# Kernel optimization log

Measured on AMD Instinct MI355X. Metric: run time of the kernel, lower is better.

The kernel has to match this reference:

```python
import jax, jax.numpy as jnp
import numpy as np

MAX_VAL = 448.0  # FP8 E4M3 max
EPS = 1e-12


def fp8_e4m3_fake_quantize(t):
    """Clamp -> per-tensor scale to E4M3 range -> power-of-two step rounding (3 mantissa bits -> step = 2^exp/8)."""
    clamped = jnp.clip(t, -MAX_VAL, MAX_VAL)
    amax = jnp.maximum(jnp.max(jnp.abs(clamped)), EPS)
    scale = MAX_VAL / amax
    scaled = clamped * scale
    sign = jnp.sign(scaled)
    mag = jnp.maximum(jnp.abs(scaled), EPS)
    exp = jnp.floor(jnp.log2(mag))
    step = jnp.exp2(exp) / 8.0
    quantized = sign * (jnp.round(mag / step) * step)
    return quantized / scale


def setup_inputs() -> dict:
    key = jax.random.key(0)
    kx, kw, kb = jax.random.split(key, 3)
    B, S, IN_F, OUT_F = 4, 2048, 4096, 16384
    x = jax.random.normal(kx, (B, S, IN_F), dtype=jnp.float32)
    weight = jax.random.normal(kw, (OUT_F, IN_F), dtype=jnp.float32) * 0.02
    bias = jax.random.normal(kb, (OUT_F,), dtype=jnp.float32) * 0.02
    return {"x": x, "weight": weight, "bias": bias}


def reference(x, weight, bias):
    w_q = fp8_e4m3_fake_quantize(weight)   # [out_f, in_f]
    x_q = fp8_e4m3_fake_quantize(x)        # [b, s, in_f]
    # F.linear: x_q @ w_q.T + bias
    return jnp.einsum('bsi,oi->bso', x_q, w_q) + bias
```

## Files before the change

### kernel.cpp

```cpp
#include <hip/hip_runtime.h>

typedef __bf16 bf16x8 __attribute__((ext_vector_type(8)));
typedef float f32x4 __attribute__((ext_vector_type(4)));

#define MAXV 448.0f

__device__ __forceinline__ void gld_lds16(const void* g, void* l) {
  __builtin_amdgcn_global_load_lds(
      (const __attribute__((address_space(1))) void*)g,
      (__attribute__((address_space(3))) void*)l, 16, 0, 0);
}

__global__ void init_ws_kernel(unsigned int* p) {
  if (threadIdx.x < 2) p[threadIdx.x] = 0u;
}

__global__ void amax_kernel(const float* __restrict__ in, long n4, unsigned int* out) {
  long i0 = (long)blockIdx.x * blockDim.x + threadIdx.x;
  long stride = (long)gridDim.x * blockDim.x;
  const float4* in4 = (const float4*)in;
  float m = 0.0f;
  for (long i = i0; i < n4; i += stride) {
    float4 v = in4[i];
    m = fmaxf(m, fmaxf(fmaxf(fabsf(v.x), fabsf(v.y)), fmaxf(fabsf(v.z), fabsf(v.w))));
  }
  m = fminf(m, MAXV);
#pragma unroll
  for (int off = 32; off >= 1; off >>= 1)
    m = fmaxf(m, __shfl_xor(m, off, 64));
  if ((threadIdx.x & 63) == 0) atomicMax(out, __float_as_uint(m));
}

__device__ __forceinline__ unsigned short fq1(float v, float scale) {
  float c = fminf(fmaxf(v, -MAXV), MAXV);
  float s = c * scale;
  float mag = fmaxf(fabsf(s), 1e-12f);
  unsigned int u = __float_as_uint(mag);
  unsigned int E = u >> 23;
  float t = __uint_as_float((u & 0x007fffffu) | (130u << 23));
  float r = rintf(t);
  float q = r * __uint_as_float((E - 3u) << 23);
  float res = (s == 0.0f) ? 0.0f : copysignf(q, s);
  return (unsigned short)(__float_as_uint(res) >> 16);
}

__global__ void quant_kernel(const float* __restrict__ in, unsigned short* __restrict__ out,
                             long n4, const unsigned int* __restrict__ amax_p) {
  float amax = fmaxf(__uint_as_float(*amax_p), 1e-12f);
  float scale = MAXV / amax;
  long i0 = (long)blockIdx.x * blockDim.x + threadIdx.x;
  long stride = (long)gridDim.x * blockDim.x;
  const float4* in4 = (const float4*)in;
  ushort4* out4 = (ushort4*)out;
  for (long i = i0; i < n4; i += stride) {
    float4 v = in4[i];
    ushort4 o;
    o.x = fq1(v.x, scale);
    o.y = fq1(v.y, scale);
    o.z = fq1(v.z, scale);
    o.w = fq1(v.w, scale);
    out4[i] = o;
  }
}

#define TM 128
#define TN 128
#define BK 32

__global__ __launch_bounds__(256, 2) void gemm_bt_kernel(
    const unsigned short* __restrict__ A, const unsigned short* __restrict__ B,
    const float* __restrict__ bias, const unsigned int* __restrict__ amax_ws,
    float* __restrict__ C, int M, int N, int K) {
  __shared__ __align__(16) unsigned short As[TM * BK];
  __shared__ __align__(16) unsigned short Bs[TN * BK];

  const int tid = threadIdx.x;
  const int lane = tid & 63;
  const int wave = tid >> 6;
  const int wm = wave >> 1, wn = wave & 1;
  const int bn = blockIdx.x, bm = blockIdx.y;

  const int mfrag = lane & 15;
  const int kq = lane >> 4;

  const int sr = tid >> 2;
  const int sc = (tid & 3) * 8;
  const unsigned short* gA0 = A + (long)(bm * TM + sr) * K + sc;
  const unsigned short* gA1 = A + (long)(bm * TM + 64 + sr) * K + sc;
  const unsigned short* gB0 = B + (long)(bn * TN + sr) * K + sc;
  const unsigned short* gB1 = B + (long)(bn * TN + 64 + sr) * K + sc;
  unsigned short* lA0 = As + tid * 8;
  unsigned short* lA1 = As + (256 + tid) * 8;
  unsigned short* lB0 = Bs + tid * 8;
  unsigned short* lB1 = Bs + (256 + tid) * 8;

  f32x4 acc[4][4] = {};

  for (int k0 = 0; k0 < K; k0 += BK) {
    __syncthreads();
    gld_lds16(gA0 + k0, lA0);
    gld_lds16(gA1 + k0, lA1);
    gld_lds16(gB0 + k0, lB0);
    gld_lds16(gB1 + k0, lB1);
    __syncthreads();

    bf16x8 af[4], bf[4];
#pragma unroll
    for (int i = 0; i < 4; ++i) {
      af[i] = *(const bf16x8*)(As + (wm * 64 + i * 16 + mfrag) * BK + kq * 8);
      bf[i] = *(const bf16x8*)(Bs + (wn * 64 + i * 16 + mfrag) * BK + kq * 8);
    }
#pragma unroll
    for (int i = 0; i < 4; ++i)
#pragma unroll
      for (int j = 0; j < 4; ++j)
        acc[i][j] = __builtin_amdgcn_mfma_f32_16x16x32_bf16(af[i], bf[j], acc[i][j], 0, 0, 0);
  }

  float amx = fmaxf(__uint_as_float(amax_ws[0]), 1e-12f);
  float amw = fmaxf(__uint_as_float(amax_ws[1]), 1e-12f);
  float sx = MAXV / amx, sw = MAXV / amw;
  float inv = 1.0f / (sx * sw);

  const int row_base = bm * TM + wm * 64 + (lane >> 4) * 4;
  const int col_base = bn * TN + wn * 64 + (lane & 15);
#pragma unroll
  for (int i = 0; i < 4; ++i)
#pragma unroll
    for (int j = 0; j < 4; ++j) {
      int col = col_base + j * 16;
      float bv = bias[col];
#pragma unroll
      for (int r = 0; r < 4; ++r) {
        int row = row_base + i * 16 + r;
        C[(long)row * N + col] = acc[i][j][r] * inv + bv;
      }
    }
}

extern "C" void kernel_launch(void* const* d_in, const int* in_sizes, int n_in,
                              void* d_out, int out_size, void* d_ws, size_t ws_size,
                              hipStream_t stream) {
  const float* x = (const float*)d_in[0];
  const float* w = (const float*)d_in[1];
  const float* bias = (const float*)d_in[2];
  float* out = (float*)d_out;

  const long NX = in_sizes[0];
  const long NW = in_sizes[1];
  const int N = in_sizes[2];
  const int K = (int)(NW / N);
  const int M = (int)(NX / K);

  unsigned int* amax = (unsigned int*)d_ws;
  unsigned short* xq = (unsigned short*)((char*)d_ws + 256);
  unsigned short* wq = (unsigned short*)((char*)d_ws + 256 + NX * 2);

  init_ws_kernel<<<1, 64, 0, stream>>>(amax);
  amax_kernel<<<1024, 256, 0, stream>>>(x, NX >> 2, amax + 0);
  amax_kernel<<<2048, 256, 0, stream>>>(w, NW >> 2, amax + 1);
  quant_kernel<<<2048, 256, 0, stream>>>(x, xq, NX >> 2, amax + 0);
  quant_kernel<<<2048, 256, 0, stream>>>(w, wq, NW >> 2, amax + 1);

  dim3 grid(N / TN, M / TM);
  gemm_bt_kernel<<<grid, 256, 0, stream>>>(xq, wq, bias, amax, out, M, N, K);
}
```

Before: 2.319 ms.

## Replace GEMM with 256x256 double-buffered, swizzled-LDS, pipelined MFMA kernel

Replaces the 128x128 single-buffered GEMM with a 256x256 tile, 512-thread kernel. It uses a 64-wide K step, XOR-swizzled LDS layout, double-buffered global-to-LDS loads interleaved with MFMA phases, setprio around compute, and an XCD-aware block remap. The aim is to raise data reuse, hide load latency behind compute and cut LDS bank conflicts. The kernel uses the full 128KB of LDS with heavy register pressure, and its many barriers and hand-tuned waitcnt counts could limit occupancy or introduce hazards.

```diff
diff --git a/kernel.cpp b/kernel.cpp
--- a/kernel.cpp
+++ b/kernel.cpp
@@ -63,78 +63,191 @@
   }
 }
 
-#define TM 128
-#define TN 128
-#define BK 32
-
-__global__ __launch_bounds__(256, 2) void gemm_bt_kernel(
+__global__ __launch_bounds__(512, 2) void gemm256_kernel(
     const unsigned short* __restrict__ A, const unsigned short* __restrict__ B,
     const float* __restrict__ bias, const unsigned int* __restrict__ amax_ws,
     float* __restrict__ C, int M, int N, int K) {
-  __shared__ __align__(16) unsigned short As[TM * BK];
-  __shared__ __align__(16) unsigned short Bs[TN * BK];
+  __shared__ __attribute__((aligned(16))) unsigned char lds[131072];
 
   const int tid = threadIdx.x;
   const int lane = tid & 63;
   const int wave = tid >> 6;
-  const int wm = wave >> 1, wn = wave & 1;
-  const int bn = blockIdx.x, bm = blockIdx.y;
-
-  const int mfrag = lane & 15;
-  const int kq = lane >> 4;
-
-  const int sr = tid >> 2;
-  const int sc = (tid & 3) * 8;
-  const unsigned short* gA0 = A + (long)(bm * TM + sr) * K + sc;
-  const unsigned short* gA1 = A + (long)(bm * TM + 64 + sr) * K + sc;
-  const unsigned short* gB0 = B + (long)(bn * TN + sr) * K + sc;
-  const unsigned short* gB1 = B + (long)(bn * TN + 64 + sr) * K + sc;
-  unsigned short* lA0 = As + tid * 8;
-  unsigned short* lA1 = As + (256 + tid) * 8;
-  unsigned short* lB0 = Bs + tid * 8;
-  unsigned short* lB1 = Bs + (256 + tid) * 8;
-
-  f32x4 acc[4][4] = {};
-
-  for (int k0 = 0; k0 < K; k0 += BK) {
-    __syncthreads();
-    gld_lds16(gA0 + k0, lA0);
-    gld_lds16(gA1 + k0, lA1);
-    gld_lds16(gB0 + k0, lB0);
-    gld_lds16(gB1 + k0, lB1);
-    __syncthreads();
-
-    bf16x8 af[4], bf[4];
-#pragma unroll
-    for (int i = 0; i < 4; ++i) {
-      af[i] = *(const bf16x8*)(As + (wm * 64 + i * 16 + mfrag) * BK + kq * 8);
-      bf[i] = *(const bf16x8*)(Bs + (wn * 64 + i * 16 + mfrag) * BK + kq * 8);
-    }
-#pragma unroll
-    for (int i = 0; i < 4; ++i)
-#pragma unroll
-      for (int j = 0; j < 4; ++j)
-        acc[i][j] = __builtin_amdgcn_mfma_f32_16x16x32_bf16(af[i], bf[j], acc[i][j], 0, 0, 0);
-  }
+  const int wm = wave >> 2, wn = wave & 3;
+  const int mfrag = lane & 15, kq = lane >> 4;
+  const int kxor = (kq * 16) ^ (((mfrag >> 3) & 1) << 5);
+
+  const int nbn = N >> 8;
+  const int wg = (blockIdx.x & 7) * (gridDim.x >> 3) + (blockIdx.x >> 3);
+  const int bm = wg / nbn, bn = wg % nbn;
+
+  const int nT = K >> 6;
+
+  const int cA0 = ((tid >> 8) << 9) + (tid & 255);
+  const int cB0 = ((tid >> 7) << 8) + (tid & 127);
+  const int cAq[2] = {cA0, cA0 + 256};
+  const int cBq[2] = {cB0, cB0 + 128};
+  const unsigned short* sA[2][2];
+  const unsigned short* sB[2][2];
+  int dA[2][2], dB[2][2];
+#pragma unroll
+  for (int q = 0; q < 2; ++q) {
+    {
+      int c = cAq[q], row = (c >> 2) & 127, kb = c >> 9, ch = c & 3;
+      int ko = kb * 32 + ((ch * 8) ^ (((row >> 3) & 1) << 4));
+#pragma unroll
+      for (int l = 0; l < 2; ++l) {
+        sA[q][l] = A + (size_t)(bm * 256 + l * 128 + row) * K + ko;
+        dA[q][l] = l * 16384 + c * 16;
+      }
+    }
+    {
+      int c = cBq[q], row = (c >> 2) & 127, kb = c >> 9, ch = c & 3;
+      int ko = kb * 32 + ((ch * 8) ^ (((row >> 3) & 1) << 4));
+#pragma unroll
+      for (int l = 0; l < 2; ++l) {
+        sB[q][l] = B + (size_t)(bn * 256 + l * 128 + row) * K + ko;
+        dB[q][l] = 32768 + l * 16384 + c * 16;
+      }
+    }
+  }
+
+#define STAGE_A(qq, T2)                                              \
+  do {                                                               \
+    long ko_ = (long)(T2) * 64;                                      \
+    int b2_ = ((T2) & 1) * 65536;                                    \
+    gld_lds16(sA[qq][0] + ko_, lds + b2_ + dA[qq][0]);               \
+    gld_lds16(sA[qq][1] + ko_, lds + b2_ + dA[qq][1]);               \
+  } while (0)
+#define STAGE_B(qq, T2)                                              \
+  do {                                                               \
+    long ko_ = (long)(T2) * 64;                                      \
+    int b2_ = ((T2) & 1) * 65536;                                    \
+    gld_lds16(sB[qq][0] + ko_, lds + b2_ + dB[qq][0]);               \
+    gld_lds16(sB[qq][1] + ko_, lds + b2_ + dB[qq][1]);               \
+  } while (0)
+
+  STAGE_A(0, 0);
+  STAGE_B(0, 0);
+  STAGE_B(1, 0);
+  STAGE_A(1, 0);
+  if (nT > 1) {
+    STAGE_A(0, 1);
+    STAGE_B(0, 1);
+    STAGE_B(1, 1);
+    asm volatile("s_waitcnt vmcnt(6)" ::: "memory");
+  } else {
+    asm volatile("s_waitcnt vmcnt(0)" ::: "memory");
+  }
+  __builtin_amdgcn_s_barrier();
+
+  const unsigned char* ldsA0 = lds + wm * 16384 + mfrag * 64 + kxor;
+  const unsigned char* ldsB0 = lds + 32768 + (wn >> 1) * 16384 + (wn & 1) * 4096 + mfrag * 64 + kxor;
+
+  f32x4 acc[8][4] = {};
+  bf16x8 af[4][2], bf[4][2];
+
+  for (int T = 0; T < nT; ++T) {
+    const unsigned char* pA = ldsA0 + (T & 1) * 65536;
+    const unsigned char* pB = ldsB0 + (T & 1) * 65536;
+
+#pragma unroll
+    for (int i = 0; i < 4; ++i)
+#pragma unroll
+      for (int ks = 0; ks < 2; ++ks)
+        af[i][ks] = *(const bf16x8*)(pA + ks * 8192 + i * 1024);
+#pragma unroll
+    for (int j = 0; j < 2; ++j)
+#pragma unroll
+      for (int ks = 0; ks < 2; ++ks)
+        bf[j][ks] = *(const bf16x8*)(pB + ks * 8192 + j * 1024);
+    if (T + 1 < nT) STAGE_A(1, T + 1);
+    __builtin_amdgcn_s_barrier();
+    __builtin_amdgcn_s_setprio(1);
+#pragma unroll
+    for (int i = 0; i < 4; ++i)
+#pragma unroll
+      for (int j = 0; j < 2; ++j) {
+        acc[i][j] = __builtin_amdgcn_mfma_f32_16x16x32_bf16(af[i][0], bf[j][0], acc[i][j], 0, 0, 0);
+        acc[i][j] = __builtin_amdgcn_mfma_f32_16x16x32_bf16(af[i][1], bf[j][1], acc[i][j], 0, 0, 0);
+      }
+    __builtin_amdgcn_s_setprio(0);
+    __builtin_amdgcn_s_barrier();
+
+#pragma unroll
+    for (int j = 2; j < 4; ++j)
+#pragma unroll
+      for (int ks = 0; ks < 2; ++ks)
+        bf[j][ks] = *(const bf16x8*)(pB + ks * 8192 + j * 1024);
+    if (T + 2 < nT) STAGE_A(0, T + 2);
+    __builtin_amdgcn_s_barrier();
+    __builtin_amdgcn_s_setprio(1);
+#pragma unroll
+    for (int i = 0; i < 4; ++i)
+#pragma unroll
+      for (int j = 2; j < 4; ++j) {
+        acc[i][j] = __builtin_amdgcn_mfma_f32_16x16x32_bf16(af[i][0], bf[j][0], acc[i][j], 0, 0, 0);
+        acc[i][j] = __builtin_amdgcn_mfma_f32_16x16x32_bf16(af[i][1], bf[j][1], acc[i][j], 0, 0, 0);
+      }
+    __builtin_amdgcn_s_setprio(0);
+    __builtin_amdgcn_s_barrier();
+
+#pragma unroll
+    for (int i = 0; i < 4; ++i)
+#pragma unroll
+      for (int ks = 0; ks < 2; ++ks)
+        af[i][ks] = *(const bf16x8*)(pA + ks * 8192 + (i + 4) * 1024);
+    if (T + 2 < nT) STAGE_B(0, T + 2);
+    __builtin_amdgcn_s_barrier();
+    __builtin_amdgcn_s_setprio(1);
+#pragma unroll
+    for (int i = 0; i < 4; ++i)
+#pragma unroll
+      for (int j = 0; j < 2; ++j) {
+        acc[i + 4][j] = __builtin_amdgcn_mfma_f32_16x16x32_bf16(af[i][0], bf[j][0], acc[i + 4][j], 0, 0, 0);
+        acc[i + 4][j] = __builtin_amdgcn_mfma_f32_16x16x32_bf16(af[i][1], bf[j][1], acc[i + 4][j], 0, 0, 0);
+      }
+    __builtin_amdgcn_s_setprio(0);
+    __builtin_amdgcn_s_barrier();
+
+    if (T + 2 < nT) STAGE_B(1, T + 2);
+    if (T < nT - 2) {
+      asm volatile("s_waitcnt vmcnt(6)" ::: "memory");
+    } else {
+      asm volatile("s_waitcnt vmcnt(0)" ::: "memory");
+    }
+    __builtin_amdgcn_s_barrier();
+    __builtin_amdgcn_s_setprio(1);
+#pragma unroll
+    for (int i = 0; i < 4; ++i)
+#pragma unroll
+      for (int j = 2; j < 4; ++j) {
+        acc[i + 4][j] = __builtin_amdgcn_mfma_f32_16x16x32_bf16(af[i][0], bf[j][0], acc[i + 4][j], 0, 0, 0);
+        acc[i + 4][j] = __builtin_amdgcn_mfma_f32_16x16x32_bf16(af[i][1], bf[j][1], acc[i + 4][j], 0, 0, 0);
+      }
+    __builtin_amdgcn_s_setprio(0);
+    __builtin_amdgcn_s_barrier();
+  }
+#undef STAGE_A
+#undef STAGE_B
 
   float amx = fmaxf(__uint_as_float(amax_ws[0]), 1e-12f);
   float amw = fmaxf(__uint_as_float(amax_ws[1]), 1e-12f);
   float sx = MAXV / amx, sw = MAXV / amw;
   float inv = 1.0f / (sx * sw);
 
-  const int row_base = bm * TM + wm * 64 + (lane >> 4) * 4;
-  const int col_base = bn * TN + wn * 64 + (lane & 15);
-#pragma unroll
-  for (int i = 0; i < 4; ++i)
+  const int rb = bm * 256 + wm * 128 + (lane >> 4) * 4;
+  const int cb = bn * 256 + wn * 64 + (lane & 15);
+  float bv[4];
+#pragma unroll
+  for (int j = 0; j < 4; ++j) bv[j] = bias[cb + j * 16];
+#pragma unroll
+  for (int i = 0; i < 8; ++i)
 #pragma unroll
     for (int j = 0; j < 4; ++j) {
-      int col = col_base + j * 16;
-      float bv = bias[col];
-#pragma unroll
-      for (int r = 0; r < 4; ++r) {
-        int row = row_base + i * 16 + r;
-        C[(long)row * N + col] = acc[i][j][r] * inv + bv;
-      }
+      const int col = cb + j * 16;
+#pragma unroll
+      for (int r = 0; r < 4; ++r)
+        C[(long)(rb + i * 16 + r) * N + col] = acc[i][j][r] * inv + bv[j];
     }
 }
 
@@ -162,6 +275,6 @@
   quant_kernel<<<2048, 256, 0, stream>>>(x, xq, NX >> 2, amax + 0);
   quant_kernel<<<2048, 256, 0, stream>>>(w, wq, NW >> 2, amax + 1);
 
-  dim3 grid(N / TN, M / TM);
-  gemm_bt_kernel<<<grid, 256, 0, stream>>>(xq, wq, bias, amax, out, M, N, K);
-}
+  dim3 grid((unsigned)((M / 256) * (N / 256)));
+  gemm256_kernel<<<grid, 512, 0, stream>>>(xq, wq, bias, amax, out, M, N, K);
+}
```

Result: faster. 1.879 ms (-18.9%).
